# Performance work log

Measured on AMD Instinct MI355X. Metric: run time of the kernel, lower is better.

The kernel has to match this reference:

```python
import jax, jax.numpy as jnp
import numpy as np

N_NODES = 50000
N_EDGES = 800000
IN_DIM = 64
HID = 64
N_CLASSES = 10
NUM_GRAPHS = 512
EPS = 1e-5


def setup_inputs() -> dict:
    key = jax.random.key(0)
    ks = jax.random.split(key, 24)
    def w(k, shape, fan_in):
        return jax.random.normal(k, shape, jnp.float32) / np.sqrt(fan_in)
    inp = {
        "input_feature": jax.random.normal(ks[0], (N_NODES, IN_DIM), jnp.float32),
        "edge_src": jax.random.randint(ks[1], (N_EDGES,), 0, N_NODES, jnp.int32),
        "edge_dst": jax.random.randint(ks[2], (N_EDGES,), 0, N_NODES, jnp.int32),
        "graph_indicator": jnp.sort(jax.random.randint(ks[3], (N_NODES,), 0, NUM_GRAPHS, jnp.int32)),
        "labels": jax.random.randint(ks[4], (NUM_GRAPHS,), 0, N_CLASSES, jnp.int32),
        # GraphSAGE layer weights (self + neighbor paths) and biases
        "Ws1": w(ks[5], (IN_DIM, HID), IN_DIM), "Wn1": w(ks[6], (IN_DIM, HID), IN_DIM), "b1": jnp.zeros((HID,), jnp.float32),
        "Ws2": w(ks[7], (HID, HID), HID), "Wn2": w(ks[8], (HID, HID), HID), "b2": jnp.zeros((HID,), jnp.float32),
        "Ws3": w(ks[9], (HID, HID), HID), "Wn3": w(ks[10], (HID, HID), HID), "b3": jnp.zeros((HID,), jnp.float32),
        # BatchNorm affine params (bn1 output is discarded by the original forward, so omitted)
        "g2": jnp.ones((HID,), jnp.float32), "be2": jnp.zeros((HID,), jnp.float32),
        "g3": jnp.ones((HID,), jnp.float32), "be3": jnp.zeros((HID,), jnp.float32),
        # MLP head
        "fcW1": w(ks[11], (HID, 2 * HID), HID), "fcb1": jnp.zeros((2 * HID,), jnp.float32),
        "fcW2": w(ks[12], (2 * HID, HID), 2 * HID), "fcb2": jnp.zeros((HID,), jnp.float32),
        "fcW3": w(ks[13], (HID, N_CLASSES), HID), "fcb3": jnp.zeros((N_CLASSES,), jnp.float32),
    }
    return inp


def _batchnorm(x, g, b):
    # training-mode BN over the node dimension
    m = jnp.mean(x, axis=0)
    v = jnp.var(x, axis=0)
    return (x - m) * jax.lax.rsqrt(v + EPS) * g + b


def _sage(x, Ws, Wn, b, src, dst, inv_deg):
    # mean-aggregate neighbor features: agg[i] = mean_{(j->i) in E} x[j]
    msg = x[src]                                                   # [E, d] gather
    agg = jax.ops.segment_sum(msg, dst, num_segments=N_NODES)       # [N, d] scatter-add
    agg = agg * inv_deg                                             # mean aggregation
    return jax.nn.relu(x @ Ws + agg @ Wn + b)


def reference(input_feature, edge_src, edge_dst, graph_indicator, labels,
              Ws1, Wn1, b1, Ws2, Wn2, b2, Ws3, Wn3, b3,
              g2, be2, g3, be3, fcW1, fcb1, fcW2, fcb2, fcW3, fcb3):
    deg = jax.ops.segment_sum(jnp.ones((N_EDGES,), jnp.float32), edge_dst, num_segments=N_NODES)
    inv_deg = (1.0 / jnp.maximum(deg, 1.0))[:, None]                # [N, 1]
    # NOTE: original forward computes bn1(input_feature) but discards it (dead code)
    h = _sage(input_feature, Ws1, Wn1, b1, edge_src, edge_dst, inv_deg)
    h = _batchnorm(h, g2, be2)
    h = _sage(h, Ws2, Wn2, b2, edge_src, edge_dst, inv_deg)
    h = _batchnorm(h, g3, be3)
    h = _sage(h, Ws3, Wn3, b3, edge_src, edge_dst, inv_deg)
    # sum-pool per graph (labels only determine the number of graphs)
    pooled = jax.ops.segment_sum(h, graph_indicator, num_segments=NUM_GRAPHS)  # [G, HID]
    h = jax.nn.relu(pooled @ fcW1 + fcb1)
    h = jax.nn.relu(h @ fcW2 + fcb2)
    logits = h @ fcW3 + fcb3                                        # [G, num_classes]
    return logits
```

## Files before the change

kernel.cpp:

```cpp
#include <hip/hip_runtime.h>

#define N_NODES   50000
#define N_EDGES   800000
#define DIM       64
#define NUM_GRAPHS 512
#define EPS       1e-5f

#define SB   1024
#define NSB  ((N_NODES + SB - 1) / SB)

__global__ void k_zero(int* __restrict__ deg, float* __restrict__ sums2,
                       float* __restrict__ sums3, float* __restrict__ pooled) {
    int i = blockIdx.x * 256 + threadIdx.x;
    if (i < N_NODES) deg[i] = 0;
    if (i < 128) { sums2[i] = 0.f; sums3[i] = 0.f; }
    if (i < NUM_GRAPHS * DIM) pooled[i] = 0.f;
}

__global__ void k_count(const int* __restrict__ dst, int* __restrict__ deg) {
    int i = blockIdx.x * 256 + threadIdx.x;
    if (i < N_EDGES) atomicAdd(&deg[dst[i]], 1);
}

__global__ void __launch_bounds__(1024)
k_scan1(const int* __restrict__ deg, int* __restrict__ bsum) {
    __shared__ int red[16];
    int t = threadIdx.x;
    int i = blockIdx.x * SB + t;
    int v = (i < N_NODES) ? deg[i] : 0;
#pragma unroll
    for (int d = 32; d; d >>= 1) v += __shfl_down(v, d, 64);
    if ((t & 63) == 0) red[t >> 6] = v;
    __syncthreads();
    if (t < 16) {
        int s = red[t];
#pragma unroll
        for (int d = 8; d; d >>= 1) s += __shfl_down(s, d, 16);
        if (t == 0) bsum[blockIdx.x] = s;
    }
}

__global__ void k_scan2(const int* __restrict__ bsum, int* __restrict__ boff) {
    int t = threadIdx.x;
    int v = (t < NSB) ? bsum[t] : 0;
    int orig = v;
#pragma unroll
    for (int d = 1; d < 64; d <<= 1) {
        int u = __shfl_up(v, d, 64);
        if (t >= d) v += u;
    }
    if (t < NSB) boff[t] = v - orig;
}

__global__ void __launch_bounds__(1024)
k_scan3(const int* __restrict__ deg, const int* __restrict__ boff,
        int* __restrict__ off, int* __restrict__ cursor, float* __restrict__ invd) {
    __shared__ int wsum[16];
    int t = threadIdx.x, lane = t & 63, w = t >> 6;
    int i = blockIdx.x * SB + t;
    int d = (i < N_NODES) ? deg[i] : 0;
    int v = d;
#pragma unroll
    for (int s = 1; s < 64; s <<= 1) {
        int u = __shfl_up(v, s, 64);
        if (lane >= s) v += u;
    }
    if (lane == 63) wsum[w] = v;
    __syncthreads();
    if (t < 16) {
        int x = wsum[t];
#pragma unroll
        for (int s = 1; s < 16; s <<= 1) {
            int u = __shfl_up(x, s, 16);
            if (t >= s) x += u;
        }
        wsum[t] = x;
    }
    __syncthreads();
    if (i < N_NODES) {
        int ex = boff[blockIdx.x] + ((w > 0) ? wsum[w - 1] : 0) + v - d;
        off[i] = ex;
        cursor[i] = ex;
        invd[i] = 1.0f / (float)max(d, 1);
        if (i == N_NODES - 1) off[N_NODES] = ex + d;
    }
}

__global__ void k_scatter(const int* __restrict__ src, const int* __restrict__ dst,
                          int* __restrict__ cursor, int* __restrict__ csr_src) {
    int i = blockIdx.x * 256 + threadIdx.x;
    if (i < N_EDGES) {
        int p = atomicAdd(&cursor[dst[i]], 1);
        csr_src[p] = src[i];
    }
}

__device__ inline unsigned short f2bf(float f) {
    unsigned u = __float_as_uint(f);
    return (unsigned short)((u + 0x7FFFu + ((u >> 16) & 1u)) >> 16);
}

#define GR 32
template<bool BN>
__global__ void __launch_bounds__(256)
k_gemm(const float* __restrict__ x, const float* __restrict__ Ws,
       const float* __restrict__ Wn, const float* __restrict__ bias,
       const float* __restrict__ bn_a, const float* __restrict__ bn_c,
       float* __restrict__ xs, unsigned short* __restrict__ xnh16) {
    __shared__ float sX[GR][DIM];
    int tid = threadIdx.x;
    int lane = tid & 63, w = tid >> 6;

    float wsr[DIM], wnr[DIM];
#pragma unroll
    for (int k = 0; k < DIM; ++k) {
        wsr[k] = Ws[k * DIM + lane];
        wnr[k] = Wn[k * DIM + lane];
    }
    float bv = bias[lane];
    float aL = 1.f, cL = 0.f;
    if constexpr (BN) { aL = bn_a[lane]; cL = bn_c[lane]; }

    int rowBase = blockIdx.x * GR;
#pragma unroll
    for (int r = 0; r < GR / 4; ++r) {
        int row = r * 4 + w;
        int gr = rowBase + row;
        float v = (gr < N_NODES) ? x[gr * DIM + lane] : 0.f;
        sX[row][lane] = fmaf(v, aL, cL);
    }
    __syncthreads();

#pragma unroll
    for (int r = 0; r < 8; ++r) {
        int row = w * 8 + r;
        float s = bv, n = 0.f;
#pragma unroll
        for (int kg = 0; kg < DIM / 4; ++kg) {
            float4 xv = *reinterpret_cast<const float4*>(&sX[row][kg * 4]);
            s = fmaf(xv.x, wsr[kg * 4 + 0], s); n = fmaf(xv.x, wnr[kg * 4 + 0], n);
            s = fmaf(xv.y, wsr[kg * 4 + 1], s); n = fmaf(xv.y, wnr[kg * 4 + 1], n);
            s = fmaf(xv.z, wsr[kg * 4 + 2], s); n = fmaf(xv.z, wnr[kg * 4 + 2], n);
            s = fmaf(xv.w, wsr[kg * 4 + 3], s); n = fmaf(xv.w, wnr[kg * 4 + 3], n);
        }
        int grow = rowBase + row;
        if (grow < N_NODES) {
            xs[grow * DIM + lane] = s;
            xnh16[grow * DIM + lane] = f2bf(n);
        }
    }
}

template<bool POOL>
__global__ void __launch_bounds__(256)
k_agg(const float* __restrict__ xs, const unsigned* __restrict__ xnh,
      const int* __restrict__ off, const int* __restrict__ csr_src,
      const float* __restrict__ inv_deg, const int* __restrict__ gind,
      float* __restrict__ h, float* __restrict__ pooled) {
    int tid = threadIdx.x;
    int w = tid >> 6;
    int lane = tid & 63;
    int hw = lane >> 5;
    int p = lane & 31;
    int half_id = blockIdx.x * 8 + w * 2 + hw;
    int rA = half_id * 2;
    int rB = rA + 1;
    int jA = off[rA], jeA = off[rA + 1];
    int jB = jeA,     jeB = off[rB + 1];
    float axA = 0.f, ayA = 0.f, axB = 0.f, ayB = 0.f;

    while (jA < jeA || jB < jeB) {
#pragma unroll
        for (int k = 0; k < 4; ++k) {
            int iA = jA + k, iB = jB + k;
            bool vA = iA < jeA, vB = iB < jeB;
            int sA = csr_src[min(iA, N_EDGES - 1)];
            int sB = csr_src[min(iB, N_EDGES - 1)];
            sA = vA ? sA : 0;
            sB = vB ? sB : 0;
            unsigned wA = xnh[sA * 32 + p];
            unsigned wB = xnh[sB * 32 + p];
            axA += vA ? __uint_as_float(wA << 16) : 0.f;
            ayA += vA ? __uint_as_float(wA & 0xFFFF0000u) : 0.f;
            axB += vB ? __uint_as_float(wB << 16) : 0.f;
            ayB += vB ? __uint_as_float(wB & 0xFFFF0000u) : 0.f;
        }
        jA += 4; jB += 4;
    }

    float idA = inv_deg[rA], idB = inv_deg[rB];
    float2 xvA = *reinterpret_cast<const float2*>(&xs[rA * DIM + 2 * p]);
    float2 xvB = *reinterpret_cast<const float2*>(&xs[rB * DIM + 2 * p]);
    float vxA = fmaxf(fmaf(axA, idA, xvA.x), 0.f);
    float vyA = fmaxf(fmaf(ayA, idA, xvA.y), 0.f);
    float vxB = fmaxf(fmaf(axB, idB, xvB.x), 0.f);
    float vyB = fmaxf(fmaf(ayB, idB, xvB.y), 0.f);
    *reinterpret_cast<float2*>(&h[rA * DIM + 2 * p]) = make_float2(vxA, vyA);
    *reinterpret_cast<float2*>(&h[rB * DIM + 2 * p]) = make_float2(vxB, vyB);
    if constexpr (POOL) {
        int gA = gind[rA], gB = gind[rB];
        atomicAdd(&pooled[gA * DIM + 2 * p], vxA);
        atomicAdd(&pooled[gA * DIM + 2 * p + 1], vyA);
        atomicAdd(&pooled[gB * DIM + 2 * p], vxB);
        atomicAdd(&pooled[gB * DIM + 2 * p + 1], vyB);
    }
}

__global__ void __launch_bounds__(256)
k_stats(const float* __restrict__ h, float* __restrict__ sums) {
    int lane = threadIdx.x & 63, w = threadIdx.x >> 6;
    float s = 0.f, q = 0.f;
    for (int r = blockIdx.x * 4 + w; r < N_NODES; r += gridDim.x * 4) {
        float v = h[r * DIM + lane];
        s += v;
        q = fmaf(v, v, q);
    }
    __shared__ float sS[4][DIM], sQ[4][DIM];
    sS[w][lane] = s; sQ[w][lane] = q;
    __syncthreads();
    if (w == 0) {
        float ts = sS[0][lane] + sS[1][lane] + sS[2][lane] + sS[3][lane];
        float tq = sQ[0][lane] + sQ[1][lane] + sQ[2][lane] + sQ[3][lane];
        atomicAdd(&sums[lane], ts);
        atomicAdd(&sums[DIM + lane], tq);
    }
}

__global__ void k_bnfin(const float* __restrict__ sums, const float* __restrict__ g,
                        const float* __restrict__ be, float* __restrict__ a,
                        float* __restrict__ c) {
    int t = threadIdx.x;
    float m = sums[t] * (1.0f / N_NODES);
    float q = sums[DIM + t] * (1.0f / N_NODES);
    float v = q - m * m;
    float inv = 1.0f / sqrtf(v + EPS);
    float av = g[t] * inv;
    a[t] = av;
    c[t] = be[t] - m * av;
}

__global__ void __launch_bounds__(128)
k_mlp(const float* __restrict__ pooled,
      const float* __restrict__ W1, const float* __restrict__ b1,
      const float* __restrict__ W2, const float* __restrict__ b2,
      const float* __restrict__ W3, const float* __restrict__ b3,
      float* __restrict__ out) {
    __shared__ float sp[64], s1[128], s2[64];
    int g = blockIdx.x, t = threadIdx.x;
    if (t < 64) sp[t] = pooled[g * 64 + t];
    __syncthreads();
    {
        float acc = b1[t];
#pragma unroll
        for (int k = 0; k < 64; ++k) acc = fmaf(sp[k], W1[k * 128 + t], acc);
        s1[t] = fmaxf(acc, 0.f);
    }
    __syncthreads();
    if (t < 64) {
        float acc = b2[t];
#pragma unroll
        for (int k = 0; k < 128; ++k) acc = fmaf(s1[k], W2[k * 64 + t], acc);
        s2[t] = fmaxf(acc, 0.f);
    }
    __syncthreads();
    if (t < 10) {
        float acc = b3[t];
#pragma unroll
        for (int k = 0; k < 64; ++k) acc = fmaf(s2[k], W3[k * 10 + t], acc);
        out[g * 10 + t] = acc;
    }
}

extern "C" void kernel_launch(void* const* d_in, const int* in_sizes, int n_in,
                              void* d_out, int out_size, void* d_ws, size_t ws_size,
                              hipStream_t stream) {
    const float* x0   = (const float*)d_in[0];
    const int* e_src  = (const int*)d_in[1];
    const int* e_dst  = (const int*)d_in[2];
    const int* gind   = (const int*)d_in[3];
    const float* Ws1 = (const float*)d_in[5],  *Wn1 = (const float*)d_in[6],  *b1 = (const float*)d_in[7];
    const float* Ws2 = (const float*)d_in[8],  *Wn2 = (const float*)d_in[9],  *b2 = (const float*)d_in[10];
    const float* Ws3 = (const float*)d_in[11], *Wn3 = (const float*)d_in[12], *b3 = (const float*)d_in[13];
    const float* g2  = (const float*)d_in[14], *be2 = (const float*)d_in[15];
    const float* g3  = (const float*)d_in[16], *be3 = (const float*)d_in[17];
    const float* fcW1 = (const float*)d_in[18], *fcb1 = (const float*)d_in[19];
    const float* fcW2 = (const float*)d_in[20], *fcb2 = (const float*)d_in[21];
    const float* fcW3 = (const float*)d_in[22], *fcb3 = (const float*)d_in[23];
    float* out = (float*)d_out;

    char* p = (char*)d_ws;
    auto carve = [&](size_t bytes) { void* r = (void*)p; p += (bytes + 255) & ~(size_t)255; return r; };
    int*   deg     = (int*)  carve(N_NODES * 4);
    int*   off     = (int*)  carve((N_NODES + 1) * 4);
    int*   cursor  = (int*)  carve(N_NODES * 4);
    int*   csr_src = (int*)  carve(N_EDGES * 4);
    float* invd    = (float*)carve(N_NODES * 4);
    int*   bsum    = (int*)  carve(NSB * 4);
    int*   boff    = (int*)  carve((NSB + 1) * 4);
    float* sums2   = (float*)carve(128 * 4);
    float* sums3   = (float*)carve(128 * 4);
    float* a2      = (float*)carve(64 * 4);
    float* c2      = (float*)carve(64 * 4);
    float* a3      = (float*)carve(64 * 4);
    float* c3      = (float*)carve(64 * 4);
    float* pooled  = (float*)carve(NUM_GRAPHS * DIM * 4);
    float* bufH    = (float*)carve((size_t)N_NODES * DIM * 4);
    float* bufXS   = (float*)carve((size_t)N_NODES * DIM * 4);
    unsigned* bufXN = (unsigned*)carve((size_t)N_NODES * 32 * 4);

    const int EB = (N_EDGES + 255) / 256;
    const int GB = (N_NODES + GR - 1) / GR;
    const int AB2 = N_NODES / 16;

    k_zero<<<(N_NODES + 255) / 256, 256, 0, stream>>>(deg, sums2, sums3, pooled);
    k_count<<<EB, 256, 0, stream>>>(e_dst, deg);
    k_scan1<<<NSB, SB, 0, stream>>>(deg, bsum);
    k_scan2<<<1, 64, 0, stream>>>(bsum, boff);
    k_scan3<<<NSB, SB, 0, stream>>>(deg, boff, off, cursor, invd);
    k_scatter<<<EB, 256, 0, stream>>>(e_src, e_dst, cursor, csr_src);

    k_gemm<false><<<GB, 256, 0, stream>>>(x0, Ws1, Wn1, b1, nullptr, nullptr,
                                          bufXS, (unsigned short*)bufXN);
    k_agg<false><<<AB2, 256, 0, stream>>>(bufXS, bufXN, off, csr_src, invd, nullptr, bufH, nullptr);

    k_stats<<<240, 256, 0, stream>>>(bufH, sums2);
    k_bnfin<<<1, 64, 0, stream>>>(sums2, g2, be2, a2, c2);
    k_gemm<true><<<GB, 256, 0, stream>>>(bufH, Ws2, Wn2, b2, a2, c2,
                                         bufXS, (unsigned short*)bufXN);
    k_agg<false><<<AB2, 256, 0, stream>>>(bufXS, bufXN, off, csr_src, invd, nullptr, bufH, nullptr);

    k_stats<<<240, 256, 0, stream>>>(bufH, sums3);
    k_bnfin<<<1, 64, 0, stream>>>(sums3, g3, be3, a3, c3);
    k_gemm<true><<<GB, 256, 0, stream>>>(bufH, Ws3, Wn3, b3, a3, c3,
                                         bufXS, (unsigned short*)bufXN);
    k_agg<true><<<AB2, 256, 0, stream>>>(bufXS, bufXN, off, csr_src, invd, gind, bufH, pooled);

    k_mlp<<<NUM_GRAPHS, 128, 0, stream>>>(pooled, fcW1, fcb1, fcW2, fcb2, fcW3, fcb3, out);
}
```

Before: 339.4 us.

## Replace atomic CSR scatter with two-pass bucketed counting sort

```diff
diff --git a/kernel.cpp b/kernel.cpp
--- a/kernel.cpp
+++ b/kernel.cpp
@@ -8,6 +8,10 @@
 
 #define SB   1024
 #define NSB  ((N_NODES + SB - 1) / SB)
+
+#define NBUCK ((N_NODES + 255) >> 8)
+#define PA_E  4096
+#define PA_B  ((N_EDGES + PA_E - 1) / PA_E)
 
 __global__ void k_zero(int* __restrict__ deg, float* __restrict__ sums2,
                        float* __restrict__ sums3, float* __restrict__ pooled) {
@@ -54,7 +58,7 @@
 
 __global__ void __launch_bounds__(1024)
 k_scan3(const int* __restrict__ deg, const int* __restrict__ boff,
-        int* __restrict__ off, int* __restrict__ cursor, float* __restrict__ invd) {
+        int* __restrict__ off, float* __restrict__ invd) {
     __shared__ int wsum[16];
     int t = threadIdx.x, lane = t & 63, w = t >> 6;
     int i = blockIdx.x * SB + t;
@@ -80,18 +84,84 @@
     if (i < N_NODES) {
         int ex = boff[blockIdx.x] + ((w > 0) ? wsum[w - 1] : 0) + v - d;
         off[i] = ex;
-        cursor[i] = ex;
         invd[i] = 1.0f / (float)max(d, 1);
         if (i == N_NODES - 1) off[N_NODES] = ex + d;
     }
 }
 
-__global__ void k_scatter(const int* __restrict__ src, const int* __restrict__ dst,
-                          int* __restrict__ cursor, int* __restrict__ csr_src) {
-    int i = blockIdx.x * 256 + threadIdx.x;
-    if (i < N_EDGES) {
-        int p = atomicAdd(&cursor[dst[i]], 1);
-        csr_src[p] = src[i];
+__global__ void k_bcinit(const int* __restrict__ off, int* __restrict__ bcur) {
+    int t = blockIdx.x * 256 + threadIdx.x;
+    if (t < NBUCK) bcur[t] = off[t << 8];
+}
+
+__global__ void __launch_bounds__(1024)
+k_passA(const int* __restrict__ src, const int* __restrict__ dst,
+        int* __restrict__ bcur, unsigned long long* __restrict__ ebuf) {
+    __shared__ int hist[NBUCK];
+    __shared__ int gbase[NBUCK];
+    int t = threadIdx.x;
+    for (int i = t; i < NBUCK; i += 1024) hist[i] = 0;
+    __syncthreads();
+    int e0 = blockIdx.x * PA_E;
+    int s0, s1, s2, s3, d0, d1, d2, d3, l0, l1, l2, l3;
+    bool v0, v1, v2, v3;
+    {
+        int e = e0 + t;
+        v0 = e < N_EDGES;
+        s0 = v0 ? src[min(e, N_EDGES - 1)] : 0;
+        d0 = v0 ? dst[min(e, N_EDGES - 1)] : 0;
+        l0 = v0 ? atomicAdd(&hist[d0 >> 8], 1) : 0;
+    }
+    {
+        int e = e0 + t + 1024;
+        v1 = e < N_EDGES;
+        s1 = v1 ? src[min(e, N_EDGES - 1)] : 0;
+        d1 = v1 ? dst[min(e, N_EDGES - 1)] : 0;
+        l1 = v1 ? atomicAdd(&hist[d1 >> 8], 1) : 0;
+    }
+    {
+        int e = e0 + t + 2048;
+        v2 = e < N_EDGES;
+        s2 = v2 ? src[min(e, N_EDGES - 1)] : 0;
+        d2 = v2 ? dst[min(e, N_EDGES - 1)] : 0;
+        l2 = v2 ? atomicAdd(&hist[d2 >> 8], 1) : 0;
+    }
+    {
+        int e = e0 + t + 3072;
+        v3 = e < N_EDGES;
+        s3 = v3 ? src[min(e, N_EDGES - 1)] : 0;
+        d3 = v3 ? dst[min(e, N_EDGES - 1)] : 0;
+        l3 = v3 ? atomicAdd(&hist[d3 >> 8], 1) : 0;
+    }
+    __syncthreads();
+    if (t < NBUCK) {
+        int h = hist[t];
+        gbase[t] = h ? atomicAdd(&bcur[t], h) : 0;
+    }
+    __syncthreads();
+    if (v0) ebuf[gbase[d0 >> 8] + l0] = ((unsigned long long)d0 << 32) | (unsigned)s0;
+    if (v1) ebuf[gbase[d1 >> 8] + l1] = ((unsigned long long)d1 << 32) | (unsigned)s1;
+    if (v2) ebuf[gbase[d2 >> 8] + l2] = ((unsigned long long)d2 << 32) | (unsigned)s2;
+    if (v3) ebuf[gbase[d3 >> 8] + l3] = ((unsigned long long)d3 << 32) | (unsigned)s3;
+}
+
+__global__ void __launch_bounds__(1024)
+k_passB(const unsigned long long* __restrict__ ebuf, const int* __restrict__ off,
+        int* __restrict__ csr_src) {
+    __shared__ int lcur[256];
+    int base = blockIdx.x << 8;
+    int nn = min(256, N_NODES - base);
+    int t = threadIdx.x;
+    if (t < nn) lcur[t] = off[base + t];
+    __syncthreads();
+    int js = off[base];
+    int je = off[base + nn];
+    for (int j = js + t; j < je; j += 1024) {
+        unsigned long long pk = ebuf[j];
+        int d = (int)(pk >> 32);
+        int s = (int)(unsigned)pk;
+        int pos = atomicAdd(&lcur[d - base], 1);
+        csr_src[pos] = s;
     }
 }
 
@@ -292,11 +362,11 @@
     auto carve = [&](size_t bytes) { void* r = (void*)p; p += (bytes + 255) & ~(size_t)255; return r; };
     int*   deg     = (int*)  carve(N_NODES * 4);
     int*   off     = (int*)  carve((N_NODES + 1) * 4);
-    int*   cursor  = (int*)  carve(N_NODES * 4);
     int*   csr_src = (int*)  carve(N_EDGES * 4);
     float* invd    = (float*)carve(N_NODES * 4);
     int*   bsum    = (int*)  carve(NSB * 4);
     int*   boff    = (int*)  carve((NSB + 1) * 4);
+    int*   bcur    = (int*)  carve(NBUCK * 4);
     float* sums2   = (float*)carve(128 * 4);
     float* sums3   = (float*)carve(128 * 4);
     float* a2      = (float*)carve(64 * 4);
@@ -307,6 +377,7 @@
     float* bufH    = (float*)carve((size_t)N_NODES * DIM * 4);
     float* bufXS   = (float*)carve((size_t)N_NODES * DIM * 4);
     unsigned* bufXN = (unsigned*)carve((size_t)N_NODES * 32 * 4);
+    unsigned long long* ebuf = (unsigned long long*)carve((size_t)N_EDGES * 8);
 
     const int EB = (N_EDGES + 255) / 256;
     const int GB = (N_NODES + GR - 1) / GR;
@@ -316,8 +387,10 @@
     k_count<<<EB, 256, 0, stream>>>(e_dst, deg);
     k_scan1<<<NSB, SB, 0, stream>>>(deg, bsum);
     k_scan2<<<1, 64, 0, stream>>>(bsum, boff);
-    k_scan3<<<NSB, SB, 0, stream>>>(deg, boff, off, cursor, invd);
-    k_scatter<<<EB, 256, 0, stream>>>(e_src, e_dst, cursor, csr_src);
+    k_scan3<<<NSB, SB, 0, stream>>>(deg, boff, off, invd);
+    k_bcinit<<<1, 256, 0, stream>>>(off, bcur);
+    k_passA<<<PA_B, 1024, 0, stream>>>(e_src, e_dst, bcur, ebuf);
+    k_passB<<<NBUCK, 1024, 0, stream>>>(ebuf, off, csr_src);
 
     k_gemm<false><<<GB, 256, 0, stream>>>(x0, Ws1, Wn1, b1, nullptr, nullptr,
                                           bufXS, (unsigned short*)bufXN);
```

After: 300.9 us. 11.3% less time.
